# Optimization experiments

Hardware: AMD Instinct MI355X
Metric: run time of the kernel (lower is better)

The kernel has to match this reference:

```python
import jax, jax.numpy as jnp
import numpy as np

IN_F = 128
OUT_F = 64
ALPHA = 0.2  # LeakyReLU slope for attention logits
NEG_INF = -9e15


def setup_inputs() -> dict:
    key = jax.random.key(0)
    k1, k2, k3, k4 = jax.random.split(key, 4)
    B, N = 4, 2048
    h = jax.random.normal(k1, (B, N, IN_F), dtype=jnp.float32)
    adj = jax.random.randint(k2, (B, N, N), 0, 2, dtype=jnp.int32)
    # xavier_uniform with gain=1.414
    def xavier(k, shape, gain=1.414):
        fan_in, fan_out = shape[0], shape[1]
        bound = gain * np.sqrt(6.0 / (fan_in + fan_out))
        return jax.random.uniform(k, shape, jnp.float32, -bound, bound)
    W = xavier(k3, (IN_F, OUT_F))
    a = xavier(k4, (2 * OUT_F, 1))
    return {"h": h, "adj": adj, "W": W, "a": a}


def reference(h, adj, W, a):
    # Wh: [B, N, F_out]
    Wh = jnp.einsum("bnf,fo->bno", h, W)
    # e_ij = LeakyReLU(a_left . Wh_i + a_right . Wh_j), avoiding the
    # O(N^2 * 2F) concatenated tensor the torch code materializes.
    a_l = a[:OUT_F, 0]   # [F_out]
    a_r = a[OUT_F:, 0]   # [F_out]
    e_l = Wh @ a_l       # [B, N]
    e_r = Wh @ a_r       # [B, N]
    e = jax.nn.leaky_relu(e_l[:, :, None] + e_r[:, None, :], ALPHA)  # [B,N,N]
    masked = jnp.where(adj > 0, e, NEG_INF)
    attention = jax.nn.softmax(masked, axis=2)
    # dropout p=0.0 (eval-mode / deterministic) -> identity
    h_prime = jax.nn.leaky_relu(jnp.einsum("bij,bjo->bio", attention, Wh), 0.01)
    return (h_prime, attention)
```

## Files before the change

kernel.cpp:

```cpp
#include <hip/hip_runtime.h>

#define NN 2048
#define BB 4
#define IN_F 128
#define OUT_F 64

typedef __attribute__((ext_vector_type(8))) short short8;
typedef __attribute__((ext_vector_type(4))) float f32x4;
typedef __attribute__((ext_vector_type(4))) int i32x4;

__device__ __forceinline__ ushort f2bf(float f) {
  uint u = __float_as_uint(f);
  uint r = (u + 0x7fffu + ((u >> 16) & 1u)) >> 16;
  return (ushort)r;
}
__device__ __forceinline__ float bf2f(ushort s) {
  return __uint_as_float(((uint)s) << 16);
}

__global__ __launch_bounds__(64) void wh_el_er_kernel(
    const float* __restrict__ h, const float* __restrict__ W,
    const float* __restrict__ a, ushort* __restrict__ Whbf,
    float* __restrict__ el, float* __restrict__ er) {
  int row = blockIdx.x;
  int o = threadIdx.x;
  const float* hr = h + (size_t)row * IN_F;
  float wh = 0.f;
  #pragma unroll 8
  for (int f = 0; f < IN_F; ++f) wh += hr[f] * W[f * OUT_F + o];
  Whbf[(size_t)row * OUT_F + o] = f2bf(wh);
  float vl = wh * a[o];
  float vr = wh * a[OUT_F + o];
  #pragma unroll
  for (int d = 32; d > 0; d >>= 1) {
    vl += __shfl_down(vl, d);
    vr += __shfl_down(vr, d);
  }
  if (o == 0) { el[row] = vl; er[row] = vr; }
}

__global__ __launch_bounds__(256) void transpose_kernel(
    const ushort* __restrict__ Whbf, ushort* __restrict__ WhbfT) {
  __shared__ uint tile[64][65];
  int b = blockIdx.x >> 5;
  int j0 = (blockIdx.x & 31) << 6;
  int t = threadIdx.x;
  int o = t & 63, jg = t >> 6;
  #pragma unroll
  for (int m = 0; m < 16; ++m) {
    int jj = jg * 16 + m;
    tile[jj][o] = (uint)Whbf[((size_t)(b * NN + j0 + jj)) * OUT_F + o];
  }
  __syncthreads();
  int oo = t >> 2, grp = t & 3;
  uint out[8];
  #pragma unroll
  for (int m = 0; m < 16; m += 2) {
    uint u0 = tile[grp * 16 + m][oo];
    uint u1 = tile[grp * 16 + m + 1][oo];
    out[m >> 1] = u0 | (u1 << 16);
  }
  uint4* dst = (uint4*)(WhbfT + ((size_t)(b * OUT_F + oo)) * NN + j0 + grp * 16);
  dst[0] = *(uint4*)&out[0];
  dst[1] = *(uint4*)&out[4];
}

__global__ __launch_bounds__(512, 4) void attn_kernel(
    const int* __restrict__ adj, const ushort* __restrict__ WhbfT,
    const float* __restrict__ el, const float* __restrict__ er,
    float* __restrict__ attn_out, float* __restrict__ hprime) {
  __shared__ __align__(16) char pbuf[16 * 4096];
  __shared__ float ers[NN];
  __shared__ float red[4][16][17];
  __shared__ float sinv[16];

  int blk = blockIdx.x;
  int b = blk >> 7;
  int i0 = (blk & 127) << 4;
  int tid = threadIdx.x;
  int wave = tid >> 6, lane = tid & 63;

  ((f32x4*)ers)[tid] = ((const f32x4*)(er + (size_t)b * NN))[tid];
  __syncthreads();

  int r0 = wave * 2, r1 = r0 + 1;
  int ia = i0 + r0, ib = i0 + r1;
  float el0 = el[(size_t)b * NN + ia];
  float el1 = el[(size_t)b * NN + ib];
  const i32x4* arow0 = (const i32x4*)(adj + ((size_t)(b * NN + ia)) * NN);
  const i32x4* arow1 = (const i32x4*)(adj + ((size_t)(b * NN + ib)) * NN);

  i32x4 a0[8], a1[8];
  #pragma unroll
  for (int it = 0; it < 8; ++it) {
    a0[it] = __builtin_nontemporal_load(&arow0[lane + 64 * it]);
    a1[it] = __builtin_nontemporal_load(&arow1[lane + 64 * it]);
  }

  uint2 pva0[8], pva1[8];
  float ss0 = 0.f, ss1 = 0.f;
  #pragma unroll
  for (int it = 0; it < 8; ++it) {
    f32x4 ev = *(const f32x4*)&ers[(lane + 64 * it) * 4];
    float evv[4] = {ev.x, ev.y, ev.z, ev.w};
    int   av0[4] = {a0[it].x, a0[it].y, a0[it].z, a0[it].w};
    int   av1[4] = {a1[it].x, a1[it].y, a1[it].z, a1[it].w};
    float pe0[4], pe1[4];
    #pragma unroll
    for (int k = 0; k < 4; ++k) {
      float e0 = el0 + evv[k];
      e0 = fmaxf(e0, 0.2f * e0);
      float x0 = __expf(e0);
      pe0[k] = av0[k] > 0 ? x0 : 0.f;
      ss0 += pe0[k];
      float e1 = el1 + evv[k];
      e1 = fmaxf(e1, 0.2f * e1);
      float x1 = __expf(e1);
      pe1[k] = av1[k] > 0 ? x1 : 0.f;
      ss1 += pe1[k];
    }
    uint2 w0, w1;
    w0.x = (uint)f2bf(pe0[0]) | ((uint)f2bf(pe0[1]) << 16);
    w0.y = (uint)f2bf(pe0[2]) | ((uint)f2bf(pe0[3]) << 16);
    w1.x = (uint)f2bf(pe1[0]) | ((uint)f2bf(pe1[1]) << 16);
    w1.y = (uint)f2bf(pe1[2]) | ((uint)f2bf(pe1[3]) << 16);
    pva0[it] = w0;
    pva1[it] = w1;
  }
  #pragma unroll
  for (int d = 32; d > 0; d >>= 1) {
    ss0 += __shfl_xor(ss0, d);
    ss1 += __shfl_xor(ss1, d);
  }
  float inv0 = 1.f / ss0, inv1 = 1.f / ss1;
  if (lane == 0) { sinv[r0] = inv0; sinv[r1] = inv1; }

  {
    f32x4* or0 = (f32x4*)(attn_out + ((size_t)(b * NN + ia)) * NN);
    f32x4* or1 = (f32x4*)(attn_out + ((size_t)(b * NN + ib)) * NN);
    #pragma unroll
    for (int it = 0; it < 8; ++it) {
      uint2 w0 = pva0[it], w1 = pva1[it];
      f32x4 v0, v1;
      v0.x = bf2f((ushort)(w0.x & 0xffff)) * inv0;
      v0.y = bf2f((ushort)(w0.x >> 16)) * inv0;
      v0.z = bf2f((ushort)(w0.y & 0xffff)) * inv0;
      v0.w = bf2f((ushort)(w0.y >> 16)) * inv0;
      or0[lane + 64 * it] = v0;
      v1.x = bf2f((ushort)(w1.x & 0xffff)) * inv1;
      v1.y = bf2f((ushort)(w1.x >> 16)) * inv1;
      v1.z = bf2f((ushort)(w1.y & 0xffff)) * inv1;
      v1.w = bf2f((ushort)(w1.y >> 16)) * inv1;
      or1[lane + 64 * it] = v1;
    }
  }

  {
    char* lr0 = pbuf + r0 * 4096;
    char* lr1 = pbuf + r1 * 4096;
    int sw0 = (r0 & 7) << 4, sw1 = (r1 & 7) << 4;
    #pragma unroll
    for (int it = 0; it < 8; ++it) {
      *(uint2*)(lr0 + (((lane + 64 * it) * 8) ^ sw0)) = pva0[it];
      *(uint2*)(lr1 + (((lane + 64 * it) * 8) ^ sw1)) = pva1[it];
    }
  }
  __syncthreads();

  int ntile = wave >> 1, khalf = wave & 1;
  int o0 = ntile * 16;
  int lo16 = lane & 15, hi4 = lane >> 4;

  const char* prowA = pbuf + lo16 * 4096;
  int swA = (lo16 & 7) << 4;
  const ushort* brow = WhbfT + ((size_t)(b * OUT_F + o0 + lo16)) * NN;

  f32x4 acc = {0.f, 0.f, 0.f, 0.f};
  #pragma unroll 8
  for (int kk = 0; kk < 32; ++kk) {
    int kbase = khalf * 1024 + kk * 32 + hi4 * 8;
    short8 afrag = *(const short8*)(prowA + ((kbase * 2) ^ swA));
    short8 bfrag = *(const short8*)(brow + kbase);
    acc = __builtin_amdgcn_mfma_f32_16x16x32_bf16(afrag, bfrag, acc, 0, 0, 0);
  }

  if (khalf == 1) {
    #pragma unroll
    for (int q = 0; q < 4; ++q) red[ntile][hi4 * 4 + q][lo16] = acc[q];
  }
  __syncthreads();
  if (khalf == 0) {
    #pragma unroll
    for (int q = 0; q < 4; ++q) {
      int crow = hi4 * 4 + q;
      float v = (acc[q] + red[ntile][crow][lo16]) * sinv[crow];
      v = v > 0.f ? v : 0.01f * v;
      hprime[((size_t)(b * NN + i0 + crow)) * OUT_F + o0 + lo16] = v;
    }
  }
}

extern "C" void kernel_launch(void* const* d_in, const int* in_sizes, int n_in,
                              void* d_out, int out_size, void* d_ws, size_t ws_size,
                              hipStream_t stream) {
  const float* h  = (const float*)d_in[0];
  const int* adj  = (const int*)d_in[1];
  const float* W  = (const float*)d_in[2];
  const float* a  = (const float*)d_in[3];

  float* hprime   = (float*)d_out;
  float* attn_out = (float*)d_out + (size_t)BB * NN * OUT_F;

  ushort* Whbf  = (ushort*)d_ws;
  ushort* WhbfT = Whbf + (size_t)BB * NN * OUT_F;
  float* el = (float*)(WhbfT + (size_t)BB * OUT_F * NN);
  float* er = el + (size_t)BB * NN;

  hipLaunchKernelGGL(wh_el_er_kernel, dim3(BB * NN), dim3(64), 0, stream,
                     h, W, a, Whbf, el, er);
  hipLaunchKernelGGL(transpose_kernel, dim3(BB * (NN / 64)), dim3(256), 0, stream,
                     Whbf, WhbfT);
  hipLaunchKernelGGL(attn_kernel, dim3(BB * (NN / 16)), dim3(512), 0, stream,
                     adj, WhbfT, el, er, attn_out, hprime);
}
```

Baseline: 58.05 us.

## Split waves into MFMA and attention-store roles after LDS staging

After the probabilities are staged in LDS, the first four waves now each compute a full 16-column output tile, using two accumulators over both K halves. This removes the cross-wave reduction buffer and its second barrier. The other four waves read the bf16 probabilities back from LDS and write the normalized fp32 attention rows, so the large attention store runs alongside the MFMA work instead of before it. The trade-off is half as many waves issuing MFMAs, and the attention store is now spread unevenly across only four waves.

```diff
diff --git a/kernel.cpp b/kernel.cpp
--- a/kernel.cpp
+++ b/kernel.cpp
@@ -71,7 +71,6 @@
     float* __restrict__ attn_out, float* __restrict__ hprime) {
   __shared__ __align__(16) char pbuf[16 * 4096];
   __shared__ float ers[NN];
-  __shared__ float red[4][16][17];
   __shared__ float sinv[16];
 
   int blk = blockIdx.x;
@@ -132,28 +131,7 @@
     ss0 += __shfl_xor(ss0, d);
     ss1 += __shfl_xor(ss1, d);
   }
-  float inv0 = 1.f / ss0, inv1 = 1.f / ss1;
-  if (lane == 0) { sinv[r0] = inv0; sinv[r1] = inv1; }
-
-  {
-    f32x4* or0 = (f32x4*)(attn_out + ((size_t)(b * NN + ia)) * NN);
-    f32x4* or1 = (f32x4*)(attn_out + ((size_t)(b * NN + ib)) * NN);
-    #pragma unroll
-    for (int it = 0; it < 8; ++it) {
-      uint2 w0 = pva0[it], w1 = pva1[it];
-      f32x4 v0, v1;
-      v0.x = bf2f((ushort)(w0.x & 0xffff)) * inv0;
-      v0.y = bf2f((ushort)(w0.x >> 16)) * inv0;
-      v0.z = bf2f((ushort)(w0.y & 0xffff)) * inv0;
-      v0.w = bf2f((ushort)(w0.y >> 16)) * inv0;
-      or0[lane + 64 * it] = v0;
-      v1.x = bf2f((ushort)(w1.x & 0xffff)) * inv1;
-      v1.y = bf2f((ushort)(w1.x >> 16)) * inv1;
-      v1.z = bf2f((ushort)(w1.y & 0xffff)) * inv1;
-      v1.w = bf2f((ushort)(w1.y >> 16)) * inv1;
-      or1[lane + 64 * it] = v1;
-    }
-  }
+  if (lane == 0) { sinv[r0] = 1.f / ss0; sinv[r1] = 1.f / ss1; }
 
   {
     char* lr0 = pbuf + r0 * 4096;
@@ -167,35 +145,51 @@
   }
   __syncthreads();
 
-  int ntile = wave >> 1, khalf = wave & 1;
-  int o0 = ntile * 16;
-  int lo16 = lane & 15, hi4 = lane >> 4;
-
-  const char* prowA = pbuf + lo16 * 4096;
-  int swA = (lo16 & 7) << 4;
-  const ushort* brow = WhbfT + ((size_t)(b * OUT_F + o0 + lo16)) * NN;
-
-  f32x4 acc = {0.f, 0.f, 0.f, 0.f};
-  #pragma unroll 8
-  for (int kk = 0; kk < 32; ++kk) {
-    int kbase = khalf * 1024 + kk * 32 + hi4 * 8;
-    short8 afrag = *(const short8*)(prowA + ((kbase * 2) ^ swA));
-    short8 bfrag = *(const short8*)(brow + kbase);
-    acc = __builtin_amdgcn_mfma_f32_16x16x32_bf16(afrag, bfrag, acc, 0, 0, 0);
-  }
-
-  if (khalf == 1) {
-    #pragma unroll
-    for (int q = 0; q < 4; ++q) red[ntile][hi4 * 4 + q][lo16] = acc[q];
-  }
-  __syncthreads();
-  if (khalf == 0) {
+  if (wave < 4) {
+    int o0 = wave * 16;
+    int lo16 = lane & 15, hi4 = lane >> 4;
+    const char* prowA = pbuf + lo16 * 4096;
+    int swA = (lo16 & 7) << 4;
+    const ushort* brow = WhbfT + ((size_t)(b * OUT_F + o0 + lo16)) * NN;
+
+    f32x4 acc0 = {0.f, 0.f, 0.f, 0.f};
+    f32x4 acc1 = {0.f, 0.f, 0.f, 0.f};
+    #pragma unroll 8
+    for (int kk = 0; kk < 32; ++kk) {
+      int ka = kk * 32 + hi4 * 8;
+      int kb = ka + 1024;
+      short8 af0 = *(const short8*)(prowA + ((ka * 2) ^ swA));
+      short8 bf0 = *(const short8*)(brow + ka);
+      acc0 = __builtin_amdgcn_mfma_f32_16x16x32_bf16(af0, bf0, acc0, 0, 0, 0);
+      short8 af1 = *(const short8*)(prowA + ((kb * 2) ^ swA));
+      short8 bf1 = *(const short8*)(brow + kb);
+      acc1 = __builtin_amdgcn_mfma_f32_16x16x32_bf16(af1, bf1, acc1, 0, 0, 0);
+    }
     #pragma unroll
     for (int q = 0; q < 4; ++q) {
       int crow = hi4 * 4 + q;
-      float v = (acc[q] + red[ntile][crow][lo16]) * sinv[crow];
+      float v = (acc0[q] + acc1[q]) * sinv[crow];
       v = v > 0.f ? v : 0.01f * v;
       hprime[((size_t)(b * NN + i0 + crow)) * OUT_F + o0 + lo16] = v;
+    }
+  } else {
+    #pragma unroll
+    for (int m = 0; m < 4; ++m) {
+      int r = (wave - 4) * 4 + m;
+      float inv = sinv[r];
+      const char* lr = pbuf + r * 4096;
+      int sw = (r & 7) << 4;
+      f32x4* orow = (f32x4*)(attn_out + ((size_t)(b * NN + i0 + r)) * NN);
+      #pragma unroll
+      for (int it = 0; it < 8; ++it) {
+        uint2 w2 = *(const uint2*)(lr + (((lane + 64 * it) * 8) ^ sw));
+        f32x4 v;
+        v.x = bf2f((ushort)(w2.x & 0xffff)) * inv;
+        v.y = bf2f((ushort)(w2.x >> 16)) * inv;
+        v.z = bf2f((ushort)(w2.y & 0xffff)) * inv;
+        v.w = bf2f((ushort)(w2.y >> 16)) * inv;
+        orow[lane + 64 * it] = v;
+      }
     }
   }
 }
```

Measured after the change: 54.02 us. 1.07x faster.

## Pack adjacency into bitmask in prep kernel and split attention store

Applied to the files above, without the earlier changes.

A prep kernel now reads the int32 adjacency once and packs it into per-row bitmasks with ballots, alongside the Wh/el/er computation. The MFMA kernel reads the compact bitmask instead of the adjacency, and the normalized attention matrix is written by a separate store kernel that recomputes the exponentials from the bits. This shrinks the working set the MFMA kernel touches and lets the large attention write run as a simple streaming kernel. In exchange it adds one kernel launch, recomputes the exp values, and leaves the adjacency read serialized in prep ahead of everything else.

```diff
diff --git a/kernel.cpp b/kernel.cpp
--- a/kernel.cpp
+++ b/kernel.cpp
@@ -18,25 +18,48 @@
   return __uint_as_float(((uint)s) << 16);
 }
 
-__global__ __launch_bounds__(64) void wh_el_er_kernel(
+
+__global__ __launch_bounds__(256) void prep_kernel(
     const float* __restrict__ h, const float* __restrict__ W,
-    const float* __restrict__ a, ushort* __restrict__ Whbf,
-    float* __restrict__ el, float* __restrict__ er) {
-  int row = blockIdx.x;
-  int o = threadIdx.x;
-  const float* hr = h + (size_t)row * IN_F;
-  float wh = 0.f;
-  #pragma unroll 8
-  for (int f = 0; f < IN_F; ++f) wh += hr[f] * W[f * OUT_F + o];
-  Whbf[(size_t)row * OUT_F + o] = f2bf(wh);
-  float vl = wh * a[o];
-  float vr = wh * a[OUT_F + o];
-  #pragma unroll
-  for (int d = 32; d > 0; d >>= 1) {
-    vl += __shfl_down(vl, d);
-    vr += __shfl_down(vr, d);
-  }
-  if (o == 0) { el[row] = vl; er[row] = vr; }
+    const float* __restrict__ a, const int* __restrict__ adj,
+    ushort* __restrict__ Whbf, float* __restrict__ el,
+    float* __restrict__ er, uint2* __restrict__ bits2) {
+  int blk = blockIdx.x;
+  int lane = threadIdx.x & 63;
+  if (blk < 2048) {
+    int row = blk * 4 + (threadIdx.x >> 6);
+    const i32x4* ar = (const i32x4*)(adj + (size_t)row * NN);
+    uint2 out; out.x = 0u; out.y = 0u;
+    #pragma unroll
+    for (int t = 0; t < 8; ++t) {
+      i32x4 v = ar[lane + 64 * t];
+      unsigned long long m0 = __ballot(v.x > 0);
+      unsigned long long m1 = __ballot(v.y > 0);
+      unsigned long long m2 = __ballot(v.z > 0);
+      unsigned long long m3 = __ballot(v.w > 0);
+      if (lane == 4 * t)     { out.x = (uint)m0; out.y = (uint)(m0 >> 32); }
+      if (lane == 4 * t + 1) { out.x = (uint)m1; out.y = (uint)(m1 >> 32); }
+      if (lane == 4 * t + 2) { out.x = (uint)m2; out.y = (uint)(m2 >> 32); }
+      if (lane == 4 * t + 3) { out.x = (uint)m3; out.y = (uint)(m3 >> 32); }
+    }
+    if (lane < 32) bits2[(size_t)row * 32 + lane] = out;
+  } else {
+    int row = (blk - 2048) * 4 + (threadIdx.x >> 6);
+    int o = threadIdx.x & 63;
+    const float* hr = h + (size_t)row * IN_F;
+    float wh = 0.f;
+    #pragma unroll 8
+    for (int f = 0; f < IN_F; ++f) wh += hr[f] * W[f * OUT_F + o];
+    Whbf[(size_t)row * OUT_F + o] = f2bf(wh);
+    float vl = wh * a[o];
+    float vr = wh * a[OUT_F + o];
+    #pragma unroll
+    for (int d = 32; d > 0; d >>= 1) {
+      vl += __shfl_down(vl, d);
+      vr += __shfl_down(vr, d);
+    }
+    if (o == 0) { el[row] = vl; er[row] = vr; }
+  }
 }
 
 __global__ __launch_bounds__(256) void transpose_kernel(
@@ -65,10 +88,10 @@
   dst[1] = *(uint4*)&out[4];
 }
 
-__global__ __launch_bounds__(512, 4) void attn_kernel(
-    const int* __restrict__ adj, const ushort* __restrict__ WhbfT,
+__global__ __launch_bounds__(512, 4) void mfma_kernel(
+    const uint2* __restrict__ bits2, const ushort* __restrict__ WhbfT,
     const float* __restrict__ el, const float* __restrict__ er,
-    float* __restrict__ attn_out, float* __restrict__ hprime) {
+    float* __restrict__ hprime) {
   __shared__ __align__(16) char pbuf[16 * 4096];
   __shared__ float ers[NN];
   __shared__ float red[4][16][17];
@@ -87,15 +110,12 @@
   int ia = i0 + r0, ib = i0 + r1;
   float el0 = el[(size_t)b * NN + ia];
   float el1 = el[(size_t)b * NN + ib];
-  const i32x4* arow0 = (const i32x4*)(adj + ((size_t)(b * NN + ia)) * NN);
-  const i32x4* arow1 = (const i32x4*)(adj + ((size_t)(b * NN + ib)) * NN);
-
-  i32x4 a0[8], a1[8];
-  #pragma unroll
-  for (int it = 0; it < 8; ++it) {
-    a0[it] = __builtin_nontemporal_load(&arow0[lane + 64 * it]);
-    a1[it] = __builtin_nontemporal_load(&arow1[lane + 64 * it]);
-  }
+  uint2 mw0 = bits2[(size_t)(b * NN + ia) * 32 + (lane & 31)];
+  uint2 mw1 = bits2[(size_t)(b * NN + ib) * 32 + (lane & 31)];
+  uint wsel0 = lane < 32 ? mw0.x : mw0.y;
+  uint wsel1 = lane < 32 ? mw1.x : mw1.y;
+  int shalf = lane & 32;
+  int bitpos = lane & 31;
 
   uint2 pva0[8], pva1[8];
   float ss0 = 0.f, ss1 = 0.f;
@@ -103,20 +123,20 @@
   for (int it = 0; it < 8; ++it) {
     f32x4 ev = *(const f32x4*)&ers[(lane + 64 * it) * 4];
     float evv[4] = {ev.x, ev.y, ev.z, ev.w};
-    int   av0[4] = {a0[it].x, a0[it].y, a0[it].z, a0[it].w};
-    int   av1[4] = {a1[it].x, a1[it].y, a1[it].z, a1[it].w};
     float pe0[4], pe1[4];
     #pragma unroll
     for (int k = 0; k < 4; ++k) {
+      uint s0 = __shfl(wsel0, 4 * it + k + shalf);
+      uint s1 = __shfl(wsel1, 4 * it + k + shalf);
       float e0 = el0 + evv[k];
       e0 = fmaxf(e0, 0.2f * e0);
       float x0 = __expf(e0);
-      pe0[k] = av0[k] > 0 ? x0 : 0.f;
+      pe0[k] = (s0 >> bitpos) & 1 ? x0 : 0.f;
       ss0 += pe0[k];
       float e1 = el1 + evv[k];
       e1 = fmaxf(e1, 0.2f * e1);
       float x1 = __expf(e1);
-      pe1[k] = av1[k] > 0 ? x1 : 0.f;
+      pe1[k] = (s1 >> bitpos) & 1 ? x1 : 0.f;
       ss1 += pe1[k];
     }
     uint2 w0, w1;
@@ -132,28 +152,7 @@
     ss0 += __shfl_xor(ss0, d);
     ss1 += __shfl_xor(ss1, d);
   }
-  float inv0 = 1.f / ss0, inv1 = 1.f / ss1;
-  if (lane == 0) { sinv[r0] = inv0; sinv[r1] = inv1; }
-
-  {
-    f32x4* or0 = (f32x4*)(attn_out + ((size_t)(b * NN + ia)) * NN);
-    f32x4* or1 = (f32x4*)(attn_out + ((size_t)(b * NN + ib)) * NN);
-    #pragma unroll
-    for (int it = 0; it < 8; ++it) {
-      uint2 w0 = pva0[it], w1 = pva1[it];
-      f32x4 v0, v1;
-      v0.x = bf2f((ushort)(w0.x & 0xffff)) * inv0;
-      v0.y = bf2f((ushort)(w0.x >> 16)) * inv0;
-      v0.z = bf2f((ushort)(w0.y & 0xffff)) * inv0;
-      v0.w = bf2f((ushort)(w0.y >> 16)) * inv0;
-      or0[lane + 64 * it] = v0;
-      v1.x = bf2f((ushort)(w1.x & 0xffff)) * inv1;
-      v1.y = bf2f((ushort)(w1.x >> 16)) * inv1;
-      v1.z = bf2f((ushort)(w1.y & 0xffff)) * inv1;
-      v1.w = bf2f((ushort)(w1.y >> 16)) * inv1;
-      or1[lane + 64 * it] = v1;
-    }
-  }
+  if (lane == 0) { sinv[r0] = 1.f / ss0; sinv[r1] = 1.f / ss1; }
 
   {
     char* lr0 = pbuf + r0 * 4096;
@@ -200,6 +199,52 @@
   }
 }
 
+__global__ __launch_bounds__(256) void store_kernel(
+    const uint2* __restrict__ bits2, const float* __restrict__ el,
+    const float* __restrict__ er, float* __restrict__ attn_out) {
+  int lane = threadIdx.x & 63;
+  int row = blockIdx.x * 4 + (threadIdx.x >> 6);
+  int b = row >> 11;
+  float eli = el[row];
+  const f32x4* er4 = (const f32x4*)(er + ((size_t)b << 11));
+  uint2 mw = bits2[(size_t)row * 32 + (lane & 31)];
+  uint wsel = lane < 32 ? mw.x : mw.y;
+  int shalf = lane & 32;
+  int bitpos = lane & 31;
+
+  float pv[8][4];
+  float ss = 0.f;
+  #pragma unroll
+  for (int it = 0; it < 8; ++it) {
+    f32x4 ev = er4[lane + 64 * it];
+    float evv[4] = {ev.x, ev.y, ev.z, ev.w};
+    #pragma unroll
+    for (int k = 0; k < 4; ++k) {
+      uint s = __shfl(wsel, 4 * it + k + shalf);
+      float e = eli + evv[k];
+      e = fmaxf(e, 0.2f * e);
+      float x = __expf(e);
+      float pe = (s >> bitpos) & 1 ? x : 0.f;
+      pv[it][k] = pe;
+      ss += pe;
+    }
+  }
+  #pragma unroll
+  for (int d = 32; d > 0; d >>= 1) ss += __shfl_xor(ss, d);
+  float inv = 1.f / ss;
+
+  f32x4* orow = (f32x4*)(attn_out + (size_t)row * NN);
+  #pragma unroll
+  for (int it = 0; it < 8; ++it) {
+    f32x4 v;
+    v.x = pv[it][0] * inv;
+    v.y = pv[it][1] * inv;
+    v.z = pv[it][2] * inv;
+    v.w = pv[it][3] * inv;
+    orow[lane + 64 * it] = v;
+  }
+}
+
 extern "C" void kernel_launch(void* const* d_in, const int* in_sizes, int n_in,
                               void* d_out, int out_size, void* d_ws, size_t ws_size,
                               hipStream_t stream) {
@@ -215,11 +260,14 @@
   ushort* WhbfT = Whbf + (size_t)BB * NN * OUT_F;
   float* el = (float*)(WhbfT + (size_t)BB * OUT_F * NN);
   float* er = el + (size_t)BB * NN;
-
-  hipLaunchKernelGGL(wh_el_er_kernel, dim3(BB * NN), dim3(64), 0, stream,
-                     h, W, a, Whbf, el, er);
+  uint2* bits2 = (uint2*)(er + (size_t)BB * NN);
+
+  hipLaunchKernelGGL(prep_kernel, dim3(4096), dim3(256), 0, stream,
+                     h, W, a, adj, Whbf, el, er, bits2);
   hipLaunchKernelGGL(transpose_kernel, dim3(BB * (NN / 64)), dim3(256), 0, stream,
                      Whbf, WhbfT);
-  hipLaunchKernelGGL(attn_kernel, dim3(BB * (NN / 16)), dim3(512), 0, stream,
-                     adj, WhbfT, el, er, attn_out, hprime);
-}
+  hipLaunchKernelGGL(mfma_kernel, dim3(BB * (NN / 16)), dim3(512), 0, stream,
+                     bits2, WhbfT, el, er, hprime);
+  hipLaunchKernelGGL(store_kernel, dim3(BB * NN / 4), dim3(256), 0, stream,
+                     bits2, el, er, attn_out);
+}
```

Result: slower. 69.97 us (+20.5%).
